# Kernel optimization log

Hardware: AMD Instinct MI355X
Metric: run time of the kernel (lower is better)

The kernel has to match this reference:

```python
import jax, jax.numpy as jnp
import numpy as np

HEADS, DIM_HEAD, LANDMARKS, PINV_ITERS = 8, 64, 256, 6


def moore_penrose_pinv(x, iters=PINV_ITERS):
    abs_x = jnp.abs(x)
    col = abs_x.sum(-1)
    row = abs_x.sum(-2)
    z = jnp.swapaxes(x, -1, -2) / (jnp.max(col) * jnp.max(row))
    I = jnp.eye(x.shape[-1], dtype=x.dtype)
    for _ in range(iters):
        xz = x @ z
        z = 0.25 * z @ (13 * I - xz @ (15 * I - xz @ (7 * I - xz)))
    return z


def nystrom_attention(x, w_qkv, w_out, b_out, res_conv_w):
    b, n, dim = x.shape
    m = LANDMARKS
    pad = (m - n % m) % m
    x = jnp.pad(x, ((0, 0), (pad, 0), (0, 0)))  # pad at front like F.pad(x,(0,0,pad,0))
    npad = n + pad
    qkv = x @ w_qkv  # (b, npad, 3*heads*dim_head)
    q, k, v = jnp.split(qkv, 3, axis=-1)
    sh = lambda t: t.reshape(b, npad, HEADS, DIM_HEAD).transpose(0, 2, 1, 3)
    q, k, v = sh(q), sh(k), sh(v)  # (b,h,npad,dh)
    q = q * (DIM_HEAD ** -0.5)
    l = npad // m
    q_l = q.reshape(b, HEADS, m, l, DIM_HEAD).mean(axis=3)  # landmarks (b,h,m,dh)
    k_l = k.reshape(b, HEADS, m, l, DIM_HEAD).mean(axis=3)
    attn1 = jax.nn.softmax(jnp.einsum('bhid,bhjd->bhij', q, k_l), -1)   # (b,h,npad,m)
    attn2 = jax.nn.softmax(jnp.einsum('bhid,bhjd->bhij', q_l, k_l), -1)  # (b,h,m,m)
    attn3 = jax.nn.softmax(jnp.einsum('bhid,bhjd->bhij', q_l, k), -1)   # (b,h,m,npad)
    out = attn1 @ (moore_penrose_pinv(attn2) @ (attn3 @ v))  # (b,h,npad,dh)
    # depthwise residual conv over sequence dim (Conv2d(heads,heads,(33,1),groups=heads,bias=False))
    res = jax.lax.conv_general_dilated(v, res_conv_w, (1, 1), ((16, 16), (0, 0)),
                                       dimension_numbers=('NCHW', 'OIHW', 'NCHW'),
                                       feature_group_count=HEADS)
    out = out + res
    out = out.transpose(0, 2, 1, 3).reshape(b, npad, HEADS * DIM_HEAD)
    out = out @ w_out + b_out
    return out[:, -n:]


def camil_forward(bag, adj_row, adj_col, adj_val, w_qkv, w_out, b_out, res_conv_w,
                  wq, wk, wv_w, wv_b, v_att, u_att, w_att, fc_kernel, fc_bias):
    N = bag.shape[1]
    # encoder
    xg = nystrom_attention(bag, w_qkv, w_out, b_out, res_conv_w)[0]  # (N,D)
    enc = xg + bag  # (1,N,D)
    q = enc @ wq  # (1,N,256)
    k = enc @ wk
    attn = jnp.einsum('bnd,bmd->bnm', q, k)[0] / jnp.sqrt(jnp.float32(256.0))  # (N,N)
    # sparse adjacency-masked neighbor aggregation
    edge_scores = adj_val * attn[adj_row, adj_col]
    A_raw = jax.ops.segment_sum(edge_scores, adj_row, num_segments=N)  # (N,)
    alpha = jax.nn.softmax(A_raw)
    value = bag @ wv_w + wv_b  # (1,N,D)
    xl = alpha[:, None] * value  # (1,N,D)
    wei2 = jax.nn.sigmoid(-xl) ** 2
    xo = xl * 2 * wei2 + 2 * enc * (1 - wei2)  # (1,N,D)
    # gated MIL attention (softmax over dim 0 of size 1, as in original)
    inst = jnp.tanh(xo @ v_att) * jax.nn.sigmoid(xo @ u_att)
    scores = inst @ w_att  # (1,N,1)
    k_alpha = jax.nn.softmax(scores, axis=0)
    attn_output = k_alpha * xo
    pooled = attn_output[0].sum(axis=0, keepdims=True)  # (1,D)
    out = pooled @ fc_kernel + fc_bias  # (1,1)
    return out, A_raw, k_alpha


def setup_inputs() -> dict:
    key = jax.random.key(0)
    ks = jax.random.split(key, 16)
    N, D, E = 10000, 512, 90000
    s = 0.02
    return {
        'bag': jax.random.normal(ks[0], (1, N, D), jnp.float32),
        'adj_row': jax.random.randint(ks[1], (E,), 0, N),
        'adj_col': jax.random.randint(ks[2], (E,), 0, N),
        'adj_val': jax.random.uniform(ks[3], (E,), jnp.float32),
        'w_qkv': jax.random.normal(ks[4], (D, 3 * HEADS * DIM_HEAD), jnp.float32) * s,
        'w_out': jax.random.normal(ks[5], (HEADS * DIM_HEAD, D), jnp.float32) * s,
        'b_out': jnp.zeros((D,), jnp.float32),
        'res_conv_w': jax.random.normal(ks[6], (HEADS, 1, 33, 1), jnp.float32) * s,
        'wq': jax.random.normal(ks[7], (D, 256), jnp.float32) * s,
        'wk': jax.random.normal(ks[8], (D, 256), jnp.float32) * s,
        'wv_w': jax.random.normal(ks[9], (D, D), jnp.float32) * s,
        'wv_b': jnp.zeros((D,), jnp.float32),
        'v_att': jax.random.normal(ks[10], (D, 128), jnp.float32) * s,
        'u_att': jax.random.normal(ks[11], (D, 128), jnp.float32) * s,
        'w_att': jax.random.normal(ks[12], (128, 1), jnp.float32) * s,
        'fc_kernel': jax.random.normal(ks[13], (D, 1), jnp.float32) * s,
        'fc_bias': jnp.zeros((1,), jnp.float32),
    }


def reference(bag, adj_row, adj_col, adj_val, w_qkv, w_out, b_out, res_conv_w,
              wq, wk, wv_w, wv_b, v_att, u_att, w_att, fc_kernel, fc_bias):
    return camil_forward(bag, adj_row, adj_col, adj_val, w_qkv, w_out, b_out, res_conv_w,
                         wq, wk, wv_w, wv_b, v_att, u_att, w_att, fc_kernel, fc_bias)
```

## Files before the change

### kernel.cpp

```cpp
#include <hip/hip_runtime.h>
#include <hip/hip_bf16.h>
#include <math.h>

#define NSEQ   10000
#define NPAD   10240
#define PADR   240
#define HEADS  8
#define DH     64
#define LM     256
#define LFAC   40
#define DMODEL 512
#define DQK    256
#define OUTSZ  20001
#define NSPLIT 16
#define KCH    128

typedef __attribute__((ext_vector_type(8))) short bf16x8;
typedef __attribute__((ext_vector_type(4))) float f32x4;
#define MFMA16(a,b,c) __builtin_amdgcn_mfma_f32_16x16x32_bf16(a,b,c,0,0,0)

typedef __attribute__((address_space(1))) const unsigned char gconst_t;
typedef __attribute__((address_space(3))) unsigned char lds_t;
#define GLD16(gp, lp) __builtin_amdgcn_global_load_lds((gconst_t*)(gp), (lds_t*)(lp), 16, 0, 0)

__device__ __forceinline__ float b2f(ushort u) {
    return __uint_as_float(((unsigned)u) << 16);
}
__device__ __forceinline__ ushort f2b(float f) {
    unsigned u = __float_as_uint(f);
    unsigned r = (u + 0x7FFFu + ((u >> 16) & 1u)) >> 16;
    return (ushort)r;
}
__device__ __forceinline__ int swz8(int bid, int nwg) {
    int q = nwg >> 3, r = nwg & 7;
    int x = bid & 7, idx = bid >> 3;
    int start = (x < r) ? x * (q + 1) : r * (q + 1) + (x - r) * q;
    return start + idx;
}
__device__ __forceinline__ f32x4 tr4(f32x4 v, int p) {
    f32x4 u, w;
    float s, r;
    s = (p & 1) ? v[0] : v[1]; r = __shfl_xor(s, 1);
    u[0] = (p & 1) ? r : v[0]; u[1] = (p & 1) ? v[1] : r;
    s = (p & 1) ? v[2] : v[3]; r = __shfl_xor(s, 1);
    u[2] = (p & 1) ? r : v[2]; u[3] = (p & 1) ? v[3] : r;
    s = (p & 2) ? u[0] : u[2]; r = __shfl_xor(s, 2);
    w[0] = (p & 2) ? r : u[0]; w[2] = (p & 2) ? u[2] : r;
    s = (p & 2) ? u[1] : u[3]; r = __shfl_xor(s, 2);
    w[1] = (p & 2) ? r : u[1]; w[3] = (p & 2) ? u[3] : r;
    return w;
}

__global__ __launch_bounds__(256)
void cvt_k(const float* __restrict__ in, ushort* __restrict__ out, int n4,
           float* __restrict__ outbuf, const float* __restrict__ fcb,
           unsigned int* __restrict__ mx)
{
    int i = blockIdx.x * 256 + threadIdx.x;
    if (i < n4) {
        float4 v = ((const float4*)in)[i];
        ushort4 u; u.x = f2b(v.x); u.y = f2b(v.y); u.z = f2b(v.z); u.w = f2b(v.w);
        ((ushort4*)out)[i] = u;
    }
    if (i == 0) { outbuf[0] = fcb[0]; mx[0] = 0u; mx[1] = 0u; }
    if (i >= 1 && i <= NSEQ) outbuf[i] = 0.f;
    if (i >= NSEQ + 1 && i < OUTSZ) outbuf[i] = 1.0f;
}

__global__ __launch_bounds__(256)
void wtrans_k(const float* __restrict__ w_qkv, const float* __restrict__ w_out,
              const float* __restrict__ wq, const float* __restrict__ wk,
              const float* __restrict__ wv_w,
              ushort* __restrict__ wqkvT, ushort* __restrict__ woutT,
              ushort* __restrict__ wqkT)
{
    __shared__ float tile[32][33];
    int g0 = blockIdx.x * 32, r0 = blockIdx.y * 32;
    const float* in; ushort* outp; int C; int lc0;
    if (g0 < 1536)      { in = w_qkv; outp = wqkvT;                      C = 1536; lc0 = g0; }
    else if (g0 < 2048) { in = w_out; outp = woutT;                      C = 512;  lc0 = g0 - 1536; }
    else if (g0 < 2304) { in = wq;    outp = wqkT;                       C = 256;  lc0 = g0 - 2048; }
    else if (g0 < 2560) { in = wk;    outp = wqkT + 256*512;             C = 256;  lc0 = g0 - 2304; }
    else                { in = wv_w;  outp = wqkvT + (size_t)1536*512;   C = 512;  lc0 = g0 - 2560; }
    int tx = threadIdx.x & 31, ty = threadIdx.x >> 5;
    for (int i = ty; i < 32; i += 8) tile[i][tx] = in[(size_t)(r0 + i) * C + lc0 + tx];
    __syncthreads();
    for (int i = ty; i < 32; i += 8) outp[(size_t)(lc0 + i) * 512 + r0 + tx] = f2b(tile[tx][i]);
}

template<int MODE, int TN>
__global__ __launch_bounds__(256)
void mgemm(const ushort* __restrict__ A, const ushort* __restrict__ Bt,
           int Mlog, int N, int K, int padr, int nbx,
           void* __restrict__ P0, void* __restrict__ P1, void* __restrict__ P2,
           void* __restrict__ P3, void* __restrict__ P4,
           const float* __restrict__ bias, const float* __restrict__ extra)
{
    constexpr int NF = TN / 32;
    constexpr int BSB = TN * 64;
    __shared__ __align__(16) char As[2 * 8192];
    __shared__ __align__(16) char Bs[2 * BSB];
    const int tid = threadIdx.x;
    const int l = tid & 63, w = tid >> 6;
    const int wm = w >> 1, wn = w & 1;
    const int wk_ = swz8(blockIdx.x, gridDim.x);
    const int row0 = (wk_ / nbx) * 128, col0 = (wk_ % nbx) * TN;
    const int lr = l & 15, lg = l >> 4;
    const bool slow = (MODE == 0) && (row0 < padr);
    const int NT = K >> 5;
    f32x4 acc[4][NF];
    #pragma unroll
    for (int i = 0; i < 4; ++i)
        #pragma unroll
        for (int j = 0; j < NF; ++j) acc[i][j] = (f32x4){0.f, 0.f, 0.f, 0.f};

    auto stage = [&](int bf, int t) {
        int k0 = t << 5;
        if (!slow) {
            #pragma unroll
            for (int c = 0; c < 2; ++c) {
                int q = w * 2 + c;
                int row = q * 16 + (l >> 2);
                GLD16(A + (size_t)(row0 + row - padr) * K + k0 + (l & 3) * 8,
                      As + bf * 8192 + q * 1024);
            }
            if (TN == 128) {
                #pragma unroll
                for (int c = 0; c < 2; ++c) {
                    int q = w * 2 + c;
                    int row = q * 16 + (l >> 2);
                    GLD16(Bt + (size_t)(col0 + row) * K + k0 + (l & 3) * 8,
                          Bs + bf * BSB + q * 1024);
                }
            } else {
                int row = w * 16 + (l >> 2);
                GLD16(Bt + (size_t)(col0 + row) * K + k0 + (l & 3) * 8,
                      Bs + bf * BSB + w * 1024);
            }
        } else {
            #pragma unroll
            for (int c = 0; c < 2; ++c) {
                int gidx = c * 256 + tid;
                int row = gidx >> 2, gr = gidx & 3;
                int phys = row0 + row - padr;
                uint4 v = {0, 0, 0, 0};
                if (phys >= 0 && phys < Mlog - padr)
                    v = *(const uint4*)(A + (size_t)phys * K + k0 + gr * 8);
                *(uint4*)(As + bf * 8192 + gidx * 16) = v;
            }
            if (TN == 128) {
                #pragma unroll
                for (int c = 0; c < 2; ++c) {
                    int gidx = c * 256 + tid;
                    int row = gidx >> 2, gr = gidx & 3;
                    *(uint4*)(Bs + bf * BSB + gidx * 16) =
                        *(const uint4*)(Bt + (size_t)(col0 + row) * K + k0 + gr * 8);
                }
            } else {
                int row = tid >> 2, gr = tid & 3;
                *(uint4*)(Bs + bf * BSB + tid * 16) =
                    *(const uint4*)(Bt + (size_t)(col0 + row) * K + k0 + gr * 8);
            }
        }
    };

    int cur = 0;
    stage(0, 0);
    __syncthreads();
    for (int t = 0; t < NT; ++t) {
        if (t + 1 < NT) stage(cur ^ 1, t + 1);
        const char* Ab = As + cur * 8192;
        const char* Bb = Bs + cur * BSB;
        bf16x8 af[4];
        #pragma unroll
        for (int mf = 0; mf < 4; ++mf)
            af[mf] = *(const bf16x8*)(Ab + (wm * 64 + mf * 16 + lr) * 64 + lg * 16);
        #pragma unroll
        for (int nf = 0; nf < NF; ++nf) {
            bf16x8 bfr = *(const bf16x8*)(Bb + (wn * (TN / 2) + nf * 16 + lr) * 64 + lg * 16);
            #pragma unroll
            for (int mf = 0; mf < 4; ++mf)
                acc[mf][nf] = MFMA16(af[mf], bfr, acc[mf][nf]);
        }
        __syncthreads();
        cur ^= 1;
    }

    const int p = lr & 3;
    #pragma unroll
    for (int mf = 0; mf < 4; ++mf)
    #pragma unroll
    for (int nf = 0; nf < NF; ++nf) {
        int cb   = col0 + wn * (TN / 2) + nf * 16 + (lr & 12);
        int rowT = row0 + wm * 64 + mf * 16 + lg * 4 + p;
        if (MODE == 0) {
            int c = col0 + wn * (TN / 2) + nf * 16 + lr;
            if ((c >> 9) == 2) {
                int hh = (c >> 6) & 7;
                int kt  = (row0 + wm * 64 + mf * 16 + lg * 4) >> 5;
                int lgp = ((mf * 2) + (lg >> 1)) & 3;
                int lanep = lr + lgp * 16;
                int e0 = (lg & 1) * 4;
                ushort4 pk;
                pk.x = f2b(acc[mf][nf][0]); pk.y = f2b(acc[mf][nf][1]);
                pk.z = f2b(acc[mf][nf][2]); pk.w = f2b(acc[mf][nf][3]);
                *(ushort4*)&((ushort*)P3)[(((size_t)hh * (NPAD/32) + kt) * 4 + (nf & 3)) * 512
                                          + lanep * 8 + e0] = pk;
            }
            int t = cb >> 9;
            f32x4 v = acc[mf][nf];
            if (t == 0) { v[0] *= 0.125f; v[1] *= 0.125f; v[2] *= 0.125f; v[3] *= 0.125f; }
            f32x4 wv = tr4(v, p);
            ushort4 pk;
            pk.x = f2b(wv[0]); pk.y = f2b(wv[1]); pk.z = f2b(wv[2]); pk.w = f2b(wv[3]);
            if (t < 3) {
                int hh = (cb >> 6) & 7, d0 = cb & 63;
                ushort* dst = (t == 0) ? (ushort*)P0 : (t == 1) ? (ushort*)P1 : (ushort*)P2;
                *(ushort4*)&dst[((size_t)hh * NPAD + rowT) * DH + d0] = pk;
            } else {
                int phys = rowT - PADR;
                if (phys >= 0)
                    *(ushort4*)&((ushort*)P4)[(size_t)phys * DMODEL + (cb & 511)] = pk;
            }
        } else if (MODE == 1) {
            f32x4 wv = tr4(acc[mf][nf], p);
            if (rowT < Mlog) {
                float4 bi = *(const float4*)(bias + cb);
                float4 ex = *(const float4*)(extra + (size_t)rowT * N + cb);
                float o0 = wv[0] + bi.x + ex.x, o1 = wv[1] + bi.y + ex.y;
                float o2 = wv[2] + bi.z + ex.z, o3 = wv[3] + bi.w + ex.w;
                *(float4*)&((float*)P0)[(size_t)rowT * N + cb] = make_float4(o0, o1, o2, o3);
                ushort4 pk; pk.x = f2b(o0); pk.y = f2b(o1); pk.z = f2b(o2); pk.w = f2b(o3);
                *(ushort4*)&((ushort*)P1)[(size_t)rowT * N + cb] = pk;
            }
        } else if (MODE == 6) {
            f32x4 wv = tr4(acc[mf][nf], p);
            if (rowT < Mlog) {
                ushort4 pk;
                pk.x = f2b(wv[0]); pk.y = f2b(wv[1]); pk.z = f2b(wv[2]); pk.w = f2b(wv[3]);
                if (cb < 256)
                    *(ushort4*)&((ushort*)P0)[(size_t)rowT * 256 + cb] = pk;
                else
                    *(ushort4*)&((ushort*)P1)[(size_t)rowT * 256 + (cb - 256)] = pk;
            }
        }
    }
}

template<bool PLAIN, bool BCI, bool WPK>
__global__ __launch_bounds__(256)
void pinv_k(const ushort* __restrict__ A, const ushort* __restrict__ Bt,
            int N, float cval, float scale,
            ushort* __restrict__ P0, ushort* __restrict__ P1)
{
    __shared__ __align__(16) char smem[49152];
    char* As = smem;
    char* Bs = smem + 16384;
    const int tid = threadIdx.x, l = tid & 63, w = tid >> 6;
    const int lr = l & 15, lg = l >> 4;
    const int col0 = blockIdx.x * 64, row0 = blockIdx.y * 32, h = blockIdx.z;
    const ushort* Ab = A + (size_t)h * 65536;
    const ushort* Btb = Bt + (size_t)h * ((size_t)N * 256);
    {
        int row = tid >> 3, seg = (tid & 7) * 64;
        const uint4* sa = (const uint4*)(Ab + (size_t)(row0 + row) * 256) + (tid & 7) * 4;
        #pragma unroll
        for (int e = 0; e < 4; ++e) {
            int off = (row * 512 + seg + e * 16) ^ ((row & 7) << 4);
            *(uint4*)(As + off) = sa[e];
        }
    }
    {
        int row = tid >> 2, seg = (tid & 3) * 128;
        const uint4* sb = (const uint4*)(Btb + (size_t)(col0 + row) * 256) + (tid & 3) * 8;
        int gn = col0 + row;
        #pragma unroll
        for (int e = 0; e < 8; ++e) {
            int off = (row * 512 + seg + e * 16) ^ ((row & 7) << 4);
            uint4 vb = sb[e];
            if (BCI) {
                union { uint4 u; ushort s[8]; } t; t.u = vb;
                int gk0 = (seg >> 1) + e * 8;
                #pragma unroll
                for (int j = 0; j < 8; ++j)
                    t.s[j] = f2b(((gn == gk0 + j) ? cval : 0.f) - b2f(t.s[j]));
                vb = t.u;
            }
            *(uint4*)(Bs + off) = vb;
        }
    }
    __syncthreads();
    f32x4 acc[2];
    acc[0] = (f32x4){0.f, 0.f, 0.f, 0.f};
    acc[1] = (f32x4){0.f, 0.f, 0.f, 0.f};
    #pragma unroll
    for (int ks = 0; ks < 8; ++ks) {
        bf16x8 af[2];
        #pragma unroll
        for (int mf = 0; mf < 2; ++mf) {
            int ar = mf * 16 + lr;
            af[mf] = *(const bf16x8*)(As + ((ar * 512 + ks * 64 + lg * 16) ^ ((ar & 7) << 4)));
        }
        int br = w * 16 + lr;
        bf16x8 bf = *(const bf16x8*)(Bs + ((br * 512 + ks * 64 + lg * 16) ^ ((br & 7) << 4)));
        acc[0] = MFMA16(af[0], bf, acc[0]);
        acc[1] = MFMA16(af[1], bf, acc[1]);
    }
    #pragma unroll
    for (int mf = 0; mf < 2; ++mf) {
        int r0v = row0 + mf * 16 + lg * 4;
        int c = col0 + w * 16 + lr;
        if (PLAIN) {
            #pragma unroll
            for (int i = 0; i < 4; ++i)
                P0[(size_t)h * 256 * N + (size_t)(r0v + i) * N + c] = f2b(acc[mf][i] * scale);
        }
        ushort4 pk;
        pk.x = f2b(acc[mf][0] * scale); pk.y = f2b(acc[mf][1] * scale);
        pk.z = f2b(acc[mf][2] * scale); pk.w = f2b(acc[mf][3] * scale);
        if (WPK) {
            int off = (((c >> 4) * 8 + (r0v >> 5)) << 9) + (((r0v >> 3) & 3) << 7)
                    + ((c & 15) << 3) + (r0v & 4);
            *(ushort4*)&P1[(size_t)h * 16384 + off] = pk;
        } else {
            *(ushort4*)&P1[(size_t)h * ((size_t)N * 256) + (size_t)c * 256 + r0v] = pk;
        }
    }
}

__global__ void landmark2_k(const ushort* __restrict__ Qb, const ushort* __restrict__ Kb,
                            ushort* __restrict__ QLb, ushort* __restrict__ KLb,
                            ushort* __restrict__ KLpk)
{
    int b = blockIdx.x;
    bool isK = b >= HEADS * LM;
    if (isK) b -= HEADS * LM;
    int hh = b >> 8, j = b & 255, d = threadIdx.x;
    const ushort* p = (isK ? Kb : Qb) + ((size_t)hh * NPAD + (size_t)j * LFAC) * DH + d;
    float s = 0.f;
    #pragma unroll
    for (int t = 0; t < LFAC; ++t) s += b2f(p[t * DH]);
    ushort u = f2b(s * (1.f / LFAC));
    (isK ? KLb : QLb)[((size_t)hh * LM + j) * DH + d] = u;
    if (isK) {
        int nf = j >> 4, lr = j & 15;
        int ks = d >> 5, lg = (d >> 3) & 3, e = d & 7;
        KLpk[(((size_t)hh * 16 + nf) * 2 + ks) * 512 + (lg * 16 + lr) * 8 + e] = u;
    }
}

__global__ __launch_bounds__(256)
void attn2_k(const ushort* __restrict__ QL, const ushort* __restrict__ KL,
             ushort* __restrict__ X2b)
{
    int i = blockIdx.x, h = blockIdx.y, j = threadIdx.x;
    __shared__ float qv[DH];
    __shared__ float red[256];
    if (j < DH) qv[j] = b2f(QL[((size_t)h * LM + i) * DH + j]);
    __syncthreads();
    const uint4* kp = (const uint4*)(KL + ((size_t)h * LM + j) * DH);
    float dot = 0.f;
    #pragma unroll
    for (int cc = 0; cc < 8; ++cc) {
        union { uint4 u; ushort s[8]; } uu; uu.u = kp[cc];
        #pragma unroll
        for (int e = 0; e < 8; ++e) dot += qv[cc * 8 + e] * b2f(uu.s[e]);
    }
    red[j] = dot; __syncthreads();
    for (int s = 128; s > 0; s >>= 1) { if (j < s) red[j] = fmaxf(red[j], red[j + s]); __syncthreads(); }
    float mx = red[0]; __syncthreads();
    float e = __expf(dot - mx);
    red[j] = e; __syncthreads();
    for (int s = 128; s > 0; s >>= 1) { if (j < s) red[j] += red[j + s]; __syncthreads(); }
    X2b[((size_t)h * LM + i) * LM + j] = f2b(e / red[0]);
}

__global__ __launch_bounds__(256)
void colrow_k(const ushort* __restrict__ X2b, unsigned int* __restrict__ mx)
{
    int h = blockIdx.x, t = threadIdx.x;
    const ushort* x = X2b + (size_t)h * LM * LM;
    float cs = 0.f, rs = 0.f;
    for (int j = 0; j < LM; ++j) cs += fabsf(b2f(x[(size_t)t * LM + j]));
    for (int i = 0; i < LM; ++i) rs += fabsf(b2f(x[(size_t)i * LM + t]));
    __shared__ float r1[256], r2[256];
    r1[t] = cs; r2[t] = rs; __syncthreads();
    for (int s = 128; s > 0; s >>= 1) {
        if (t < s) { r1[t] = fmaxf(r1[t], r1[t + s]); r2[t] = fmaxf(r2[t], r2[t + s]); }
        __syncthreads();
    }
    if (t == 0) {
        atomicMax(&mx[0], __float_as_uint(r1[0]));
        atomicMax(&mx[1], __float_as_uint(r2[0]));
    }
}

__global__ void zinit_k(const ushort* __restrict__ X2b, const float* __restrict__ mxf,
                        ushort* __restrict__ Z, ushort* __restrict__ Zt)
{
    int i = blockIdx.x, h = blockIdx.y, j = threadIdx.x;
    float scale = 1.f / (mxf[0] * mxf[1]);
    float x = b2f(X2b[((size_t)h * LM + i) * LM + j]) * scale;
    ushort u = f2b(x);
    Z[((size_t)h * LM + j) * LM + i] = u;
    Zt[((size_t)h * LM + i) * LM + j] = u;
}

__global__ __launch_bounds__(256)
void attn3_fa(const ushort* __restrict__ QLb, const ushort* __restrict__ Kb,
              const ushort* __restrict__ VtPk,
              float* __restrict__ Opart, float* __restrict__ Mpart,
              float* __restrict__ Lpart)
{
    __shared__ __align__(16) char smem[9216 + 18432];
    ushort* Qs = (ushort*)smem;
    ushort* Ks = (ushort*)(smem + 9216);
    ushort* Ps = (ushort*)(smem + 9216);
    const int tid = threadIdx.x, l = tid & 63, wv = tid >> 6;
    const int split = blockIdx.x, qt = blockIdx.y, h = blockIdx.z;
    const int lr = l & 15, lg = l >> 4;
    {
        int row = tid >> 2, seg = (tid & 3) * 16;
        const uint4* src = (const uint4*)(QLb + ((size_t)h * LM + qt * 64 + row) * DH + seg);
        *(uint4*)&Qs[row * 72 + seg] = src[0];
        *(uint4*)&Qs[row * 72 + seg + 8] = src[1];
    }
    f32x4 o[4];
    float m_[4], l_[4];
    #pragma unroll
    for (int nf = 0; nf < 4; ++nf) o[nf] = (f32x4){0.f, 0.f, 0.f, 0.f};
    #pragma unroll
    for (int i = 0; i < 4; ++i) { m_[i] = -INFINITY; l_[i] = 0.f; }
    const int k0base = split * (NPAD / NSPLIT);
    for (int ch = 0; ch < NPAD / NSPLIT / KCH; ++ch) {
        int kg0 = k0base + ch * KCH;
        __syncthreads();
        {
            int row = tid >> 1, half = (tid & 1) * 32;
            const uint4* src = (const uint4*)(Kb + ((size_t)h * NPAD + kg0 + row) * DH + half);
            #pragma unroll
            for (int e = 0; e < 4; ++e) *(uint4*)&Ks[row * 72 + half + e * 8] = src[e];
        }
        __syncthreads();
        f32x4 s[8];
        #pragma unroll
        for (int nf = 0; nf < 8; ++nf) s[nf] = (f32x4){0.f, 0.f, 0.f, 0.f};
        #pragma unroll
        for (int ks = 0; ks < 2; ++ks) {
            bf16x8 a = *(const bf16x8*)&Qs[(wv * 16 + lr) * 72 + ks * 32 + lg * 8];
            #pragma unroll
            for (int nf = 0; nf < 8; ++nf) {
                bf16x8 b = *(const bf16x8*)&Ks[(nf * 16 + lr) * 72 + ks * 32 + lg * 8];
                s[nf] = MFMA16(a, b, s[nf]);
            }
        }
        float scl[4];
        #pragma unroll
        for (int i = 0; i < 4; ++i) {
            float mx = s[0][i];
            #pragma unroll
            for (int nf = 1; nf < 8; ++nf) mx = fmaxf(mx, s[nf][i]);
            mx = fmaxf(mx, __shfl_xor(mx, 1)); mx = fmaxf(mx, __shfl_xor(mx, 2));
            mx = fmaxf(mx, __shfl_xor(mx, 4)); mx = fmaxf(mx, __shfl_xor(mx, 8));
            float mn = fmaxf(m_[i], mx);
            float sum = 0.f;
            #pragma unroll
            for (int nf = 0; nf < 8; ++nf) {
                float e = __expf(s[nf][i] - mn); s[nf][i] = e; sum += e;
            }
            sum += __shfl_xor(sum, 1); sum += __shfl_xor(sum, 2);
            sum += __shfl_xor(sum, 4); sum += __shfl_xor(sum, 8);
            float sc = __expf(m_[i] - mn);
            l_[i] = l_[i] * sc + sum;
            m_[i] = mn;
            scl[i] = sc;
        }
        #pragma unroll
        for (int nf = 0; nf < 4; ++nf)
        #pragma unroll
        for (int i = 0; i < 4; ++i) o[nf][i] *= scl[i];
        __syncthreads();
        #pragma unroll
        for (int nf = 0; nf < 8; ++nf)
        #pragma unroll
        for (int i = 0; i < 4; ++i) {
            int row = wv * 16 + lg * 4 + i;
            int col = nf * 16 + lr;
            Ps[row * 128 + (col ^ ((row & 7) << 3))] = f2b(s[nf][i]);
        }
        #pragma unroll
        for (int ks = 0; ks < 4; ++ks) {
            int row = wv * 16 + lr;
            int kcol = ks * 32 + lg * 8;
            bf16x8 a = *(const bf16x8*)&Ps[row * 128 + (kcol ^ ((row & 7) << 3))];
            int kgt = (kg0 >> 5) + ks;
            #pragma unroll
            for (int nf = 0; nf < 4; ++nf) {
                bf16x8 b = *(const bf16x8*)(VtPk +
                    (((size_t)h * (NPAD/32) + kgt) * 4 + nf) * 512 + (size_t)l * 8);
                o[nf] = MFMA16(a, b, o[nf]);
            }
        }
    }
    const int base = (split * 4 + qt) * 8 + h;
    #pragma unroll
    for (int nf = 0; nf < 4; ++nf)
    #pragma unroll
    for (int i = 0; i < 4; ++i) {
        int r = wv * 16 + lg * 4 + i;
        int c = nf * 16 + lr;
        Opart[((size_t)base * 64 + r) * 64 + c] = o[nf][i];
    }
    if (lr == 0) {
        #pragma unroll
        for (int i = 0; i < 4; ++i) {
            int r = wv * 16 + lg * 4 + i;
            Mpart[base * 64 + r] = m_[i];
            Lpart[base * 64 + r] = l_[i];
        }
    }
}

__global__ __launch_bounds__(256)
void mergeAV_k(const float* __restrict__ Opart, const float* __restrict__ Mpart,
               const float* __restrict__ Lpart, ushort* __restrict__ AVt)
{
    int qt = blockIdx.x, h = blockIdx.y, rq = blockIdx.z;
    int t = threadIdx.x;
    int r = rq * 32 + (t >> 3), c0 = (t & 7) * 8;
    float mv[NSPLIT];
    float mstar = -INFINITY;
    #pragma unroll
    for (int s = 0; s < NSPLIT; ++s) {
        mv[s] = Mpart[((s * 4 + qt) * 8 + h) * 64 + r];
        mstar = fmaxf(mstar, mv[s]);
    }
    float wgt[NSPLIT];
    float L = 0.f;
    #pragma unroll
    for (int s = 0; s < NSPLIT; ++s) {
        wgt[s] = __expf(mv[s] - mstar);
        L += wgt[s] * Lpart[((s * 4 + qt) * 8 + h) * 64 + r];
    }
    float inv = 1.f / L;
    float acc[8] = {};
    #pragma unroll
    for (int s = 0; s < NSPLIT; ++s) {
        const float* op = Opart + (((size_t)(s * 4 + qt) * 8 + h) * 64 + r) * 64 + c0;
        #pragma unroll
        for (int e = 0; e < 8; ++e) acc[e] += wgt[s] * op[e];
    }
    #pragma unroll
    for (int e = 0; e < 8; ++e)
        AVt[((size_t)h * DH + c0 + e) * LM + qt * 64 + r] = f2b(acc[e] * inv);
}

__global__ __launch_bounds__(256)
void conv_k(const ushort* __restrict__ Vb, const float* __restrict__ cw,
            ushort* __restrict__ OBc)
{
    int idx = blockIdx.x * 256 + threadIdx.x;
    if (idx >= NSEQ * 128) return;
    int ro = idx >> 7, c4 = idx & 127;
    int h = c4 >> 4, dq = (c4 & 15) * 4;
    int i = ro + PADR;
    float a0 = 0, a1 = 0, a2 = 0, a3 = 0;
    #pragma unroll
    for (int tt = 0; tt < 33; ++tt) {
        int src = i + tt - 16;
        if (src < NPAD) {
            float wv = cw[h * 33 + tt];
            ushort4 u = *(const ushort4*)(Vb + ((size_t)h * NPAD + src) * DH + dq);
            a0 += wv * b2f(u.x); a1 += wv * b2f(u.y);
            a2 += wv * b2f(u.z); a3 += wv * b2f(u.w);
        }
    }
    ushort4 o; o.x = f2b(a0); o.y = f2b(a1); o.z = f2b(a2); o.w = f2b(a3);
    *(ushort4*)&OBc[(size_t)ro * DMODEL + h * DH + dq] = o;
}

__global__ __launch_bounds__(256, 4)
void outrows64v2(const ushort* __restrict__ Qb, const ushort* __restrict__ KLpk,
                 const ushort* __restrict__ Wpk, const ushort* __restrict__ OBc,
                 ushort* __restrict__ OBb)
{
    __shared__ __align__(16) char smem[40960];
    char*   Qs  = smem;
    ushort* KLs = (ushort*)(smem + 8192);
    ushort* Ps  = (ushort*)(smem + 8192);
    const int tid = threadIdx.x, l = tid & 63, w = tid >> 6;
    const int h = blockIdx.y, i0 = blockIdx.x * 64;
    const int lr = l & 15, lg = l >> 4;

    ushort obc[4][4];
    #pragma unroll
    for (int nf = 0; nf < 4; ++nf)
    #pragma unroll
    for (int i = 0; i < 4; ++i) {
        int r = i0 + w * 16 + lg * 4 + i;
        obc[nf][i] = (r >= PADR)
            ? OBc[(size_t)(r - PADR) * DMODEL + h * DH + nf * 16 + lr] : (ushort)0;
    }
    {
        int row = tid >> 2;
        int seg = (tid & 3) * 32;
        const uint4* src = (const uint4*)(Qb + ((size_t)h * NPAD + i0 + row) * DH) + (tid & 3) * 2;
        uint4 v0 = src[0], v1 = src[1];
        int sw = (row & 7) << 4;
        *(uint4*)(Qs + row * 128 + (seg ^ sw)) = v0;
        *(uint4*)(Qs + row * 128 + ((seg + 16) ^ sw)) = v1;
    }
    {
        const uint4* src = (const uint4*)(KLpk + (size_t)h * 16384) + tid;
        uint4* dst = (uint4*)KLs + tid;
        #pragma unroll
        for (int e = 0; e < 8; ++e) dst[e * 256] = src[e * 256];
    }
    __syncthreads();

    f32x4 s[16];
    #pragma unroll
    for (int nf = 0; nf < 16; ++nf) s[nf] = (f32x4){0.f, 0.f, 0.f, 0.f};
    #pragma unroll
    for (int ks = 0; ks < 2; ++ks) {
        int qrow = w * 16 + lr;
        bf16x8 a = *(const bf16x8*)(Qs + qrow * 128 +
                                    ((ks * 64 + lg * 16) ^ ((qrow & 7) << 4)));
        #pragma unroll
        for (int nf = 0; nf < 16; ++nf) {
            bf16x8 b = *(const bf16x8*)&KLs[((nf * 2 + ks) * 64 + l) * 8];
            s[nf] = MFMA16(a, b, s[nf]);
        }
    }
    float inv_[4];
    #pragma unroll
    for (int i = 0; i < 4; ++i) {
        float m = s[0][i];
        #pragma unroll
        for (int nf = 1; nf < 16; ++nf) m = fmaxf(m, s[nf][i]);
        m = fmaxf(m, __shfl_xor(m, 1)); m = fmaxf(m, __shfl_xor(m, 2));
        m = fmaxf(m, __shfl_xor(m, 4)); m = fmaxf(m, __shfl_xor(m, 8));
        float sum = 0.f;
        #pragma unroll
        for (int nf = 0; nf < 16; ++nf) {
            float e = __expf(s[nf][i] - m); s[nf][i] = e; sum += e;
        }
        sum += __shfl_xor(sum, 1); sum += __shfl_xor(sum, 2);
        sum += __shfl_xor(sum, 4); sum += __shfl_xor(sum, 8);
        inv_[i] = 1.f / sum;
    }
    __syncthreads();
    #pragma unroll
    for (int nf = 0; nf < 16; ++nf)
    #pragma unroll
    for (int i = 0; i < 4; ++i) {
        int row = w * 16 + lg * 4 + i;
        int col = nf * 16 + lr;
        Ps[row * 256 + (col ^ ((row & 7) << 3))] = f2b(s[nf][i] * inv_[i]);
    }
    f32x4 o[4];
    #pragma unroll
    for (int nf = 0; nf < 4; ++nf) o[nf] = (f32x4){0.f, 0.f, 0.f, 0.f};
    #pragma unroll
    for (int ks = 0; ks < 8; ++ks) {
        int row = w * 16 + lr;
        int kcol = ks * 32 + lg * 8;
        bf16x8 a = *(const bf16x8*)&Ps[row * 256 + (kcol ^ ((row & 7) << 3))];
        #pragma unroll
        for (int nf = 0; nf < 4; ++nf) {
            bf16x8 b = *(const bf16x8*)(Wpk + (((size_t)h * 2048) + nf * 512 + ks * 64 + l) * 8);
            o[nf] = MFMA16(a, b, o[nf]);
        }
    }
    #pragma unroll
    for (int nf = 0; nf < 4; ++nf)
    #pragma unroll
    for (int i = 0; i < 4; ++i) {
        int r = i0 + w * 16 + lg * 4 + i;
        if (r >= PADR) {
            int ro = r - PADR;
            int c = h * DH + nf * 16 + lr;
            OBb[(size_t)ro * DMODEL + c] = f2b(o[nf][i] + b2f(obc[nf][i]));
        }
    }
}

__global__ __launch_bounds__(256)
void edges_k(const int* __restrict__ rows, const int* __restrict__ cols,
             const float* __restrict__ vals,
             const ushort* __restrict__ QE, const ushort* __restrict__ KE,
             float* __restrict__ A_raw, int E)
{
    int gid = blockIdx.x * blockDim.x + threadIdx.x;
    int e = gid >> 4, l = gid & 15;
    if (e >= E) return;
    int r = rows[e], c = cols[e];
    const uint4* qp = (const uint4*)(QE + (size_t)r * DQK + l * 16);
    const uint4* kp = (const uint4*)(KE + (size_t)c * DQK + l * 16);
    float dot = 0.f;
    #pragma unroll
    for (int g = 0; g < 2; ++g) {
        union { uint4 u; ushort s[8]; } qq, kk;
        qq.u = qp[g]; kk.u = kp[g];
        #pragma unroll
        for (int j = 0; j < 8; ++j) dot += b2f(qq.s[j]) * b2f(kk.s[j]);
    }
    dot += __shfl_xor(dot, 8); dot += __shfl_xor(dot, 4);
    dot += __shfl_xor(dot, 2); dot += __shfl_xor(dot, 1);
    if (l == 0) atomicAdd(&A_raw[r], vals[e] * dot * 0.0625f);
}

__global__ __launch_bounds__(1024)
void alphasm_k(const float* __restrict__ A_raw, float* __restrict__ alpha)
{
    __shared__ float red[1024];
    int t = threadIdx.x;
    float lm = -INFINITY;
    for (int i = t; i < NSEQ; i += 1024) lm = fmaxf(lm, A_raw[i]);
    red[t] = lm; __syncthreads();
    for (int s = 512; s > 0; s >>= 1) { if (t < s) red[t] = fmaxf(red[t], red[t + s]); __syncthreads(); }
    float mx = red[0]; __syncthreads();
    float ls = 0.f;
    for (int i = t; i < NSEQ; i += 1024) ls += __expf(A_raw[i] - mx);
    red[t] = ls; __syncthreads();
    for (int s = 512; s > 0; s >>= 1) { if (t < s) red[t] += red[t + s]; __syncthreads(); }
    float inv = 1.f / red[0];
    for (int i = t; i < NSEQ; i += 1024) alpha[i] = __expf(A_raw[i] - mx) * inv;
}

__global__ __launch_bounds__(256)
void xo_pooled_k(const ushort* __restrict__ VALb, const float* __restrict__ ENCf,
                 const float* __restrict__ alpha, const float* __restrict__ wvb,
                 const float* __restrict__ fck, float* __restrict__ out0)
{
    __shared__ float red[256];
    int t = threadIdx.x;
    float acc = 0.f;
    const int total = NSEQ * 128;
    for (int idx = blockIdx.x * 256 + t; idx < total; idx += gridDim.x * 256) {
        int r = idx >> 7, dq = (idx & 127) * 4;
        float al = alpha[r];
        ushort4 v4 = *(const ushort4*)(VALb + (size_t)r * DMODEL + dq);
        float4 e4 = *(const float4*)(ENCf + (size_t)r * DMODEL + dq);
        float4 b4 = *(const float4*)(wvb + dq);
        float4 f4 = *(const float4*)(fck + dq);
        float vv[4] = {b2f(v4.x) + b4.x, b2f(v4.y) + b4.y,
                       b2f(v4.z) + b4.z, b2f(v4.w) + b4.w};
        float ee[4] = {e4.x, e4.y, e4.z, e4.w};
        float ff[4] = {f4.x, f4.y, f4.z, f4.w};
        #pragma unroll
        for (int j = 0; j < 4; ++j) {
            float xl = al * vv[j];
            float s = 1.f / (1.f + __expf(xl));
            float w2 = s * s;
            float xo = 2.f * xl * w2 + 2.f * ee[j] * (1.f - w2);
            acc += xo * ff[j];
        }
    }
    red[t] = acc; __syncthreads();
    for (int s = 128; s > 0; s >>= 1) { if (t < s) red[t] += red[t + s]; __syncthreads(); }
    if (t == 0) atomicAdd(out0, red[0]);
}

extern "C" void kernel_launch(void* const* d_in, const int* in_sizes, int n_in,
                              void* d_out, int out_size, void* d_ws, size_t ws_size,
                              hipStream_t stream)
{
    (void)n_in; (void)out_size; (void)ws_size;
    const float* bag   = (const float*)d_in[0];
    const int*   arow  = (const int*)d_in[1];
    const int*   acol  = (const int*)d_in[2];
    const float* aval  = (const float*)d_in[3];
    const float* w_qkv = (const float*)d_in[4];
    const float* w_out = (const float*)d_in[5];
    const float* b_out = (const float*)d_in[6];
    const float* convw = (const float*)d_in[7];
    const float* wq    = (const float*)d_in[8];
    const float* wk    = (const float*)d_in[9];
    const float* wv_w  = (const float*)d_in[10];
    const float* wv_b  = (const float*)d_in[11];
    const float* fck   = (const float*)d_in[15];
    const float* fcb   = (const float*)d_in[16];
    const int E = in_sizes[1];
    float* out = (float*)d_out;

    char* ws = (char*)d_ws;
    size_t off = 0;
    auto alloc = [&](size_t bytes) { void* p = ws + off; off += (bytes + 255) & ~(size_t)255; return p; };
    ushort* Qb    = (ushort*)alloc((size_t)HEADS * NPAD * DH * 2);
    ushort* Kb    = (ushort*)alloc((size_t)HEADS * NPAD * DH * 2);
    ushort* Vb    = (ushort*)alloc((size_t)HEADS * NPAD * DH * 2);
    ushort* bagb  = (ushort*)alloc((size_t)NSEQ * DMODEL * 2);
    ushort* wqkvT = (ushort*)alloc((size_t)2048 * 512 * 2);
    ushort* woutT = (ushort*)alloc((size_t)512 * 512 * 2);
    ushort* wqkT  = (ushort*)alloc((size_t)512 * 512 * 2);
    ushort* VALb  = (ushort*)alloc((size_t)NSEQ * DMODEL * 2);
    ushort* QLb   = (ushort*)alloc((size_t)HEADS * LM * DH * 2);
    ushort* KLb   = (ushort*)alloc((size_t)HEADS * LM * DH * 2);
    ushort* KLpk  = (ushort*)alloc((size_t)HEADS * LM * DH * 2);
    ushort* Wpk   = (ushort*)alloc((size_t)HEADS * DH * LM * 2);
    ushort* X2b   = (ushort*)alloc((size_t)HEADS * LM * LM * 2);
    ushort* Za    = (ushort*)alloc((size_t)HEADS * LM * LM * 2);
    ushort* Zat   = (ushort*)alloc((size_t)HEADS * LM * LM * 2);
    ushort* Zb2   = (ushort*)alloc((size_t)HEADS * LM * LM * 2);
    ushort* Zbt2  = (ushort*)alloc((size_t)HEADS * LM * LM * 2);
    ushort* T0    = (ushort*)alloc((size_t)HEADS * LM * LM * 2);
    ushort* T0t   = (ushort*)alloc((size_t)HEADS * LM * LM * 2);
    ushort* T1t   = (ushort*)alloc((size_t)HEADS * LM * LM * 2);
    ushort* T2t   = (ushort*)alloc((size_t)HEADS * LM * LM * 2);
    ushort* AVt   = (ushort*)alloc((size_t)HEADS * DH * LM * 2);
    ushort* OBc   = (ushort*)alloc((size_t)NSEQ * DMODEL * 2);
    ushort* OBb   = (ushort*)alloc((size_t)NSEQ * DMODEL * 2);
    float*  ENCf  = (float*)alloc((size_t)NSEQ * DMODEL * 4);
    ushort* ENCb  = (ushort*)alloc((size_t)NSEQ * DMODEL * 2);
    float*  ALPHA = (float*)alloc((size_t)NPAD * 4);
    float*  MXf   = (float*)alloc(256);
    unsigned int* MX = (unsigned int*)MXf;
    ushort* QEb = Qb;
    ushort* KEb = Kb;
    ushort* VtPk  = (ushort*)ENCf;
    float*  Opart = (float*)ENCb;
    float*  Mpart = (float*)((char*)ENCb + 8388608);
    float*  Lpart = (float*)((char*)ENCb + 8519680);

    cvt_k<<<(NSEQ * DMODEL / 4 + 255) / 256, 256, 0, stream>>>(
        bag, bagb, NSEQ * DMODEL / 4, out, fcb, MX);
    wtrans_k<<<dim3(96, 16), 256, 0, stream>>>(w_qkv, w_out, wq, wk, wv_w,
                                               wqkvT, woutT, wqkT);

    mgemm<0, 128><<<1280, 256, 0, stream>>>(
        bagb, wqkvT, NPAD, 2048, 512, PADR, 16,
        Qb, Kb, Vb, VtPk, VALb, nullptr, nullptr);

    landmark2_k<<<2 * HEADS * LM, DH, 0, stream>>>(Qb, Kb, QLb, KLb, KLpk);

    attn2_k<<<dim3(LM, HEADS), 256, 0, stream>>>(QLb, KLb, X2b);
    colrow_k<<<HEADS, 256, 0, stream>>>(X2b, MX);
    zinit_k<<<dim3(LM, HEADS), 256, 0, stream>>>(X2b, MXf, Za, Zat);

    ushort *Z = Za, *Zt = Zat, *Zn = Zb2, *Znt = Zbt2;
    for (int it = 0; it < 6; ++it) {
        pinv_k<true,  false, false><<<dim3(4, 8, HEADS), 256, 0, stream>>>(
            X2b, Zt, LM, 0.f, 1.f, T0, T0t);
        pinv_k<false, true,  false><<<dim3(4, 8, HEADS), 256, 0, stream>>>(
            T0, T0t, LM, 7.f, 1.f, nullptr, T1t);
        pinv_k<false, true,  false><<<dim3(4, 8, HEADS), 256, 0, stream>>>(
            T0, T1t, LM, 15.f, 1.f, nullptr, T2t);
        pinv_k<true,  true,  false><<<dim3(4, 8, HEADS), 256, 0, stream>>>(
            Z, T2t, LM, 13.f, 0.25f, Zn, Znt);
        ushort* t;
        t = Z; Z = Zn; Zn = t;
        t = Zt; Zt = Znt; Znt = t;
    }

    attn3_fa<<<dim3(NSPLIT, 4, HEADS), 256, 0, stream>>>(QLb, Kb, VtPk, Opart, Mpart, Lpart);
    mergeAV_k<<<dim3(4, HEADS, 2), 256, 0, stream>>>(Opart, Mpart, Lpart, AVt);
    pinv_k<false, false, true><<<dim3(1, 8, HEADS), 256, 0, stream>>>(
        Za, AVt, DH, 0.f, 1.f, nullptr, Wpk);

    conv_k<<<(NSEQ * 128 + 255) / 256, 256, 0, stream>>>(Vb, convw, OBc);
    outrows64v2<<<dim3(NPAD / 64, HEADS), 256, 0, stream>>>(Qb, KLpk, Wpk, OBc, OBb);

    mgemm<1, 64><<<632, 256, 0, stream>>>(
        OBb, woutT, NSEQ, DMODEL, 512, 0, 8,
        ENCf, ENCb, nullptr, nullptr, nullptr, b_out, bag);

    mgemm<6, 64><<<632, 256, 0, stream>>>(
        ENCb, wqkT, NSEQ, 512, 512, 0, 8,
        QEb, KEb, nullptr, nullptr, nullptr, nullptr, nullptr);

    edges_k<<<(E * 16 + 255) / 256, 256, 0, stream>>>(arow, acol, aval, QEb, KEb, out + 1, E);
    alphasm_k<<<1, 1024, 0, stream>>>(out + 1, ALPHA);

    xo_pooled_k<<<1280, 256, 0, stream>>>(VALb, ENCf, ALPHA, wv_b, fck, out);
}
```

Baseline: 352.6 us.

## Refactor Newton-Schulz pinv iteration into three GEMM launches via algebraic expansion

Expands the iteration z·(13I − xz(15I − xz(7I − xz))) so that each step needs only three matrix multiplies: T0 = xz, then P·(7I−P) and Z·P computed in one launch, then (Z·P)·(P(7I−P)) combined with Z and Z·P elementwise. This removes one dependent GEMM launch per iteration, cutting launch count and serialization across the six iterations. The changed summation order in bf16 may alter numerical error slightly. The identity subtraction is fused into the tile load.

```diff
diff --git a/kernel.cpp b/kernel.cpp
--- a/kernel.cpp
+++ b/kernel.cpp
@@ -325,6 +325,149 @@
         } else {
             *(ushort4*)&P1[(size_t)h * ((size_t)N * 256) + (size_t)c * 256 + r0v] = pk;
         }
+    }
+}
+
+__global__ __launch_bounds__(256)
+void ns2_k(const ushort* __restrict__ P, const ushort* __restrict__ Pt,
+           const ushort* __restrict__ Z,
+           ushort* __restrict__ Qt, ushort* __restrict__ V1)
+{
+    __shared__ __align__(16) char smem[49152];
+    char* As = smem;
+    char* Bs = smem + 16384;
+    const int tid = threadIdx.x, l = tid & 63, w = tid >> 6;
+    const int lr = l & 15, lg = l >> 4;
+    const int col0 = blockIdx.x * 64;
+    const int which = blockIdx.y >> 3;
+    const int row0 = (blockIdx.y & 7) * 32;
+    const int h = blockIdx.z;
+    const ushort* Ab = (which ? Z : P) + (size_t)h * 65536;
+    const ushort* Btb = Pt + (size_t)h * 65536;
+    {
+        int row = tid >> 3, seg = (tid & 7) * 64;
+        const uint4* sa = (const uint4*)(Ab + (size_t)(row0 + row) * 256) + (tid & 7) * 4;
+        #pragma unroll
+        for (int e = 0; e < 4; ++e) {
+            int off = (row * 512 + seg + e * 16) ^ ((row & 7) << 4);
+            *(uint4*)(As + off) = sa[e];
+        }
+    }
+    {
+        int row = tid >> 2, seg = (tid & 3) * 128;
+        const uint4* sb = (const uint4*)(Btb + (size_t)(col0 + row) * 256) + (tid & 3) * 8;
+        int gn = col0 + row;
+        #pragma unroll
+        for (int e = 0; e < 8; ++e) {
+            int off = (row * 512 + seg + e * 16) ^ ((row & 7) << 4);
+            uint4 vb = sb[e];
+            if (which == 0) {
+                union { uint4 u; ushort s[8]; } t; t.u = vb;
+                int gk0 = (seg >> 1) + e * 8;
+                #pragma unroll
+                for (int j = 0; j < 8; ++j)
+                    t.s[j] = f2b(((gn == gk0 + j) ? 7.f : 0.f) - b2f(t.s[j]));
+                vb = t.u;
+            }
+            *(uint4*)(Bs + off) = vb;
+        }
+    }
+    __syncthreads();
+    f32x4 acc[2];
+    acc[0] = (f32x4){0.f, 0.f, 0.f, 0.f};
+    acc[1] = (f32x4){0.f, 0.f, 0.f, 0.f};
+    #pragma unroll
+    for (int ks = 0; ks < 8; ++ks) {
+        bf16x8 af[2];
+        #pragma unroll
+        for (int mf = 0; mf < 2; ++mf) {
+            int ar = mf * 16 + lr;
+            af[mf] = *(const bf16x8*)(As + ((ar * 512 + ks * 64 + lg * 16) ^ ((ar & 7) << 4)));
+        }
+        int br = w * 16 + lr;
+        bf16x8 bf = *(const bf16x8*)(Bs + ((br * 512 + ks * 64 + lg * 16) ^ ((br & 7) << 4)));
+        acc[0] = MFMA16(af[0], bf, acc[0]);
+        acc[1] = MFMA16(af[1], bf, acc[1]);
+    }
+    #pragma unroll
+    for (int mf = 0; mf < 2; ++mf) {
+        int r0v = row0 + mf * 16 + lg * 4;
+        int c = col0 + w * 16 + lr;
+        if (which == 0) {
+            ushort4 pk;
+            pk.x = f2b(acc[mf][0]); pk.y = f2b(acc[mf][1]);
+            pk.z = f2b(acc[mf][2]); pk.w = f2b(acc[mf][3]);
+            *(ushort4*)&Qt[(size_t)h * 65536 + (size_t)c * 256 + r0v] = pk;
+        } else {
+            #pragma unroll
+            for (int i = 0; i < 4; ++i)
+                V1[(size_t)h * 65536 + (size_t)(r0v + i) * 256 + c] = f2b(acc[mf][i]);
+        }
+    }
+}
+
+__global__ __launch_bounds__(256)
+void ns3_k(const ushort* __restrict__ V1, const ushort* __restrict__ Qt,
+           const ushort* __restrict__ Z,
+           ushort* __restrict__ Zn, ushort* __restrict__ Znt)
+{
+    __shared__ __align__(16) char smem[49152];
+    char* As = smem;
+    char* Bs = smem + 16384;
+    const int tid = threadIdx.x, l = tid & 63, w = tid >> 6;
+    const int lr = l & 15, lg = l >> 4;
+    const int col0 = blockIdx.x * 64, row0 = blockIdx.y * 32, h = blockIdx.z;
+    const ushort* Ab = V1 + (size_t)h * 65536;
+    const ushort* Btb = Qt + (size_t)h * 65536;
+    {
+        int row = tid >> 3, seg = (tid & 7) * 64;
+        const uint4* sa = (const uint4*)(Ab + (size_t)(row0 + row) * 256) + (tid & 7) * 4;
+        #pragma unroll
+        for (int e = 0; e < 4; ++e) {
+            int off = (row * 512 + seg + e * 16) ^ ((row & 7) << 4);
+            *(uint4*)(As + off) = sa[e];
+        }
+    }
+    {
+        int row = tid >> 2, seg = (tid & 3) * 128;
+        const uint4* sb = (const uint4*)(Btb + (size_t)(col0 + row) * 256) + (tid & 3) * 8;
+        #pragma unroll
+        for (int e = 0; e < 8; ++e) {
+            int off = (row * 512 + seg + e * 16) ^ ((row & 7) << 4);
+            *(uint4*)(Bs + off) = sb[e];
+        }
+    }
+    __syncthreads();
+    f32x4 acc[2];
+    acc[0] = (f32x4){0.f, 0.f, 0.f, 0.f};
+    acc[1] = (f32x4){0.f, 0.f, 0.f, 0.f};
+    #pragma unroll
+    for (int ks = 0; ks < 8; ++ks) {
+        bf16x8 af[2];
+        #pragma unroll
+        for (int mf = 0; mf < 2; ++mf) {
+            int ar = mf * 16 + lr;
+            af[mf] = *(const bf16x8*)(As + ((ar * 512 + ks * 64 + lg * 16) ^ ((ar & 7) << 4)));
+        }
+        int br = w * 16 + lr;
+        bf16x8 bf = *(const bf16x8*)(Bs + ((br * 512 + ks * 64 + lg * 16) ^ ((br & 7) << 4)));
+        acc[0] = MFMA16(af[0], bf, acc[0]);
+        acc[1] = MFMA16(af[1], bf, acc[1]);
+    }
+    #pragma unroll
+    for (int mf = 0; mf < 2; ++mf) {
+        int r0v = row0 + mf * 16 + lg * 4;
+        int c = col0 + w * 16 + lr;
+        ushort4 pk;
+        #pragma unroll
+        for (int i = 0; i < 4; ++i) {
+            size_t idx = (size_t)h * 65536 + (size_t)(r0v + i) * 256 + c;
+            float o = 0.25f * acc[mf][i] + 3.25f * b2f(Z[idx]) - 3.75f * b2f(V1[idx]);
+            ushort u = f2b(o);
+            Zn[idx] = u;
+            ((ushort*)&pk)[i] = u;
+        }
+        *(ushort4*)&Znt[(size_t)h * 65536 + (size_t)c * 256 + r0v] = pk;
     }
 }
 
@@ -840,14 +983,10 @@
 
     ushort *Z = Za, *Zt = Zat, *Zn = Zb2, *Znt = Zbt2;
     for (int it = 0; it < 6; ++it) {
-        pinv_k<true,  false, false><<<dim3(4, 8, HEADS), 256, 0, stream>>>(
+        pinv_k<true, false, false><<<dim3(4, 8, HEADS), 256, 0, stream>>>(
             X2b, Zt, LM, 0.f, 1.f, T0, T0t);
-        pinv_k<false, true,  false><<<dim3(4, 8, HEADS), 256, 0, stream>>>(
-            T0, T0t, LM, 7.f, 1.f, nullptr, T1t);
-        pinv_k<false, true,  false><<<dim3(4, 8, HEADS), 256, 0, stream>>>(
-            T0, T1t, LM, 15.f, 1.f, nullptr, T2t);
-        pinv_k<true,  true,  false><<<dim3(4, 8, HEADS), 256, 0, stream>>>(
-            Z, T2t, LM, 13.f, 0.25f, Zn, Znt);
+        ns2_k<<<dim3(4, 16, HEADS), 256, 0, stream>>>(T0, T0t, Z, T1t, T2t);
+        ns3_k<<<dim3(4, 8, HEADS), 256, 0, stream>>>(T2t, T1t, Z, Zn, Znt);
         ushort* t;
         t = Z; Z = Zn; Zn = t;
         t = Zt; Zt = Znt; Znt = t;
```

After: 350.8 us. About the same (-0.5%).
